# Kernel tuning notes

Measured on AMD Instinct MI355X. Metric: run time of the kernel, lower is better.

## Reference

```python
import jax, jax.numpy as jnp
import numpy as np

PAD_IDX = 0  # tgt_dict.stoi[PAD_WORD]
TLEN, BATCH, SLEN, CVOCAB = 64, 32, 128, 64
D, VOCAB = 1024, 50257


def setup_inputs() -> dict:
    key = jax.random.key(0)
    ks = jax.random.split(key, 7)
    hidden = jax.random.normal(ks[0], (TLEN * BATCH, D), dtype=jnp.float32)
    # attention distribution over source positions (rows sum to 1)
    attn = jax.nn.softmax(jax.random.normal(ks[1], (TLEN * BATCH, SLEN), dtype=jnp.float32), axis=-1)
    # sparse one-hot indicator: each source position maps to one extended-vocab slot
    src_idx = jax.random.randint(ks[2], (SLEN, BATCH), 0, CVOCAB)
    src_map = jax.nn.one_hot(src_idx, CVOCAB, dtype=jnp.float32)  # [slen, batch, cvocab]
    W_gen = jax.random.normal(ks[3], (VOCAB, D), dtype=jnp.float32) * 0.02
    b_gen = jnp.zeros((VOCAB,), dtype=jnp.float32)
    W_copy = jax.random.normal(ks[4], (1, D), dtype=jnp.float32) * 0.02
    b_copy = jnp.zeros((1,), dtype=jnp.float32)
    return {"hidden": hidden, "attn": attn, "src_map": src_map,
            "W_gen": W_gen, "b_gen": b_gen, "W_copy": W_copy, "b_copy": b_copy}


def reference(hidden, attn, src_map, W_gen, b_gen, W_copy, b_copy):
    slen, batch, cvocab = src_map.shape
    # p_softmax over tgt dict, with PAD masked to -inf before softmax
    logits = hidden @ W_gen.T + b_gen                      # [N, vocab]
    logits = logits.at[:, PAD_IDX].set(-jnp.inf)
    prob = jax.nn.softmax(logits, axis=-1)                 # [N, vocab]
    # copy gate p(z)
    p_copy = jax.nn.sigmoid(hidden @ W_copy.T + b_copy)    # [N, 1]
    out_prob = prob * (1.0 - p_copy)                       # [N, vocab]
    mul_attn = attn * p_copy                               # [N, slen]
    # torch flattening is tlen-major: view(-1, batch, slen) -> [tlen, batch, slen]
    mul_attn = mul_attn.reshape(-1, batch, slen)
    # bmm against sparse one-hot indicator: [tlen,batch,slen] x [slen,batch,cvocab]
    copy_prob = jnp.einsum('tbs,sbc->tbc', mul_attn, src_map)
    copy_prob = copy_prob.reshape(-1, cvocab)              # [N, cvocab]
    return jnp.concatenate([out_prob, copy_prob], axis=1)  # [N, vocab+cvocab]
```

## Files before the change

### kernel.cpp

```cpp
#include <hip/hip_runtime.h>
#include <hip/hip_bf16.h>

#define VOCAB 50257
#define CVOCAB 64
#define OUTW (VOCAB + CVOCAB)
#define DDIM 1024
#define NROWS 2048
#define SLEN 128
#define NVT 393
#define NVT2 197
#define VOCABP2 (NVT2 * 256)

typedef __attribute__((ext_vector_type(8))) short bf16x8;
typedef __attribute__((ext_vector_type(4))) float f32x4;

__device__ __forceinline__ unsigned short f2bf(float f) {
  union { float f; unsigned u; } x; x.f = f;
  unsigned r = x.u + 0x7FFFu + ((x.u >> 16) & 1u);
  return (unsigned short)(r >> 16);
}

__device__ __forceinline__ unsigned char f2e4m3(float f) {
  unsigned u = __float_as_uint(f);
  unsigned s = (u >> 24) & 0x80u;
  float a = __uint_as_float(u & 0x7FFFFFFFu);
  if (!(a < 448.f)) a = 448.f;
  if (a < 0.015625f) {
    int q = (int)rintf(a * 512.f);
    return (unsigned char)(s | (unsigned)q);
  }
  unsigned b = __float_as_uint(a);
  unsigned lsb = (b >> 20) & 1u;
  b += 0x0007FFFFu + lsb;
  int e = (int)((b >> 23) & 0xFF) - 127;
  unsigned m = (b >> 20) & 7u;
  return (unsigned char)(s | ((unsigned)(e + 7) << 3) | m);
}

__device__ __forceinline__ unsigned pack_e4m3x4(float a, float b, float c, float d) {
#if __has_builtin(__builtin_amdgcn_cvt_pk_fp8_f32)
  int r = __builtin_amdgcn_cvt_pk_fp8_f32(a, b, 0, false);
  r = __builtin_amdgcn_cvt_pk_fp8_f32(c, d, r, true);
  return (unsigned)r;
#else
  return (unsigned)f2e4m3(a) | ((unsigned)f2e4m3(b) << 8) |
         ((unsigned)f2e4m3(c) << 16) | ((unsigned)f2e4m3(d) << 24);
#endif
}

__device__ __forceinline__ void gload_lds16(const void* g, void* l) {
  __builtin_amdgcn_global_load_lds((const __attribute__((address_space(1))) void*)g,
                                   (__attribute__((address_space(3))) void*)l, 16, 0, 0);
}

__global__ __launch_bounds__(256) void k_pcopy(const float* __restrict__ hidden,
                                               const float* __restrict__ Wc,
                                               const float* __restrict__ bc,
                                               float* __restrict__ pc) {
  int n = blockIdx.x * 4 + (threadIdx.x >> 6);
  int lane = threadIdx.x & 63;
  const float4* h = (const float4*)(hidden + (size_t)n * DDIM);
  const float4* w = (const float4*)Wc;
  float s = 0.0f;
  for (int i = lane; i < DDIM / 4; i += 64) {
    float4 a = h[i], b = w[i];
    s += a.x * b.x + a.y * b.y + a.z * b.z + a.w * b.w;
  }
  #pragma unroll
  for (int m = 1; m < 64; m <<= 1) s += __shfl_xor(s, m);
  if (lane == 0) pc[n] = 1.0f / (1.0f + __expf(-(s + bc[0])));
}

__global__ __launch_bounds__(256) void k_cvtA8(const float* __restrict__ src,
                                               unsigned char* __restrict__ dst) {
  int i = blockIdx.x * 256 + threadIdx.x;
  float4 v = *(const float4*)(src + (size_t)i * 4);
  *(unsigned*)(dst + (size_t)i * 4) = pack_e4m3x4(v.x, v.y, v.z, v.w);
}

__global__ __launch_bounds__(256) void k_cvtW8(const float* __restrict__ Wg,
                                               unsigned char* __restrict__ Wf8) {
  int row = blockIdx.x;
  int t = threadIdx.x;
  unsigned r = 0;
  if (row < VOCAB) {
    float4 v = *(const float4*)(Wg + (size_t)row * DDIM + t * 4);
    r = pack_e4m3x4(v.x * 64.f, v.y * 64.f, v.z * 64.f, v.w * 64.f);
  }
  *(unsigned*)(Wf8 + (size_t)row * DDIM + t * 4) = r;
}

template<int OM>
__global__ __launch_bounds__(512, 2) void k_gemm8(const unsigned char* __restrict__ A,
                                                  const unsigned char* __restrict__ W,
                                                  const float* __restrict__ bg,
                                                  float* __restrict__ out,
                                                  unsigned short* __restrict__ ebuf,
                                                  float* __restrict__ partial) {
  __shared__ __align__(16) unsigned char sA[2][2][256 * 32];
  __shared__ __align__(16) unsigned char sB[2][2][256 * 32];

  const int tid = threadIdx.x;
  const int lane = tid & 63;
  const int w = tid >> 6;
  const int wr = w >> 2, wn = w & 3;
  const int lrow = lane & 15, kgrp = lane >> 4;

  int swz = (blockIdx.x & 7) * 197 + (blockIdx.x >> 3);
  const int mt = swz & 7, vt = swz >> 3;
  const int m0 = mt * 256;
  const int v0 = vt * 256;

  const int srow = tid >> 1, sc16 = tid & 1;
  const int c16s = sc16 ^ ((srow >> 2) & 1);

  #define STAGE_A(t, s) \
    gload_lds16(A + (size_t)(m0 + srow) * DDIM + (t) * 64 + (s) * 32 + c16s * 16, \
                &sA[(t) & 1][s][(size_t)tid * 16]);
  #define STAGE_B(t, s) \
    gload_lds16(W + (size_t)(v0 + srow) * DDIM + (t) * 64 + (s) * 32 + c16s * 16, \
                &sB[(t) & 1][s][(size_t)tid * 16]);

  int aoff[8], boff[4];
  #pragma unroll
  for (int rf = 0; rf < 8; rf++) {
    int row = wr * 128 + rf * 16 + lrow;
    aoff[rf] = row * 32 + (((kgrp >> 1) ^ ((row >> 2) & 1)) << 4) + ((kgrp & 1) << 3);
  }
  #pragma unroll
  for (int cf = 0; cf < 4; cf++) {
    int row = wn * 64 + cf * 16 + lrow;
    boff[cf] = row * 32 + (((kgrp >> 1) ^ ((row >> 2) & 1)) << 4) + ((kgrp & 1) << 3);
  }

  f32x4 acc[8][4] = {};

  STAGE_A(0, 0); STAGE_B(0, 0);
  STAGE_A(0, 1); STAGE_B(0, 1);
  STAGE_A(1, 0); STAGE_B(1, 0);
  asm volatile("s_waitcnt vmcnt(4)" ::: "memory");
  __builtin_amdgcn_s_barrier();

  #define PHASE2(t, sg, STAGE_STMT, WAIT_STMT) { \
    const int _buf = (t) & 1; \
    unsigned long af[8], bfr[4]; \
    const unsigned char* pa = &sA[_buf][sg][0]; \
    const unsigned char* pb = &sB[_buf][sg][0]; \
    _Pragma("unroll") \
    for (int rf = 0; rf < 8; rf++) \
      af[rf] = *(const unsigned long*)(pa + aoff[rf]); \
    _Pragma("unroll") \
    for (int cf = 0; cf < 4; cf++) \
      bfr[cf] = *(const unsigned long*)(pb + boff[cf]); \
    STAGE_STMT; \
    __builtin_amdgcn_s_setprio(1); \
    _Pragma("unroll") \
    for (int rf = 0; rf < 8; rf++) \
      _Pragma("unroll") \
      for (int cf = 0; cf < 4; cf++) \
        acc[rf][cf] = __builtin_amdgcn_mfma_f32_16x16x32_fp8_fp8( \
            (long)af[rf], (long)bfr[cf], acc[rf][cf], 0, 0, 0); \
    __builtin_amdgcn_s_setprio(0); \
    WAIT_STMT; \
    __builtin_amdgcn_s_barrier(); \
  }

  for (int t = 0; t < 16; t++) {
    PHASE2(t, 0,
      { if (t < 15) { STAGE_A(t + 1, 1); STAGE_B(t + 1, 1); } },
      { if (t < 15) { asm volatile("s_waitcnt vmcnt(4)" ::: "memory"); }
        else        { asm volatile("s_waitcnt vmcnt(0)" ::: "memory"); } });
    PHASE2(t, 1,
      { if (t < 14) { STAGE_A(t + 2, 0); STAGE_B(t + 2, 0); } },
      { if (t < 14)       { asm volatile("s_waitcnt vmcnt(4)" ::: "memory"); }
        else if (t == 14) { asm volatile("s_waitcnt vmcnt(2)" ::: "memory"); } });
  }

  asm volatile("s_waitcnt vmcnt(0)" ::: "memory");
  __syncthreads();
  float* psum = (float*)&sA[0][0][0];

  const float INV = 0.015625f;
  float bgv[4];
  int vcol[4];
  #pragma unroll
  for (int cf = 0; cf < 4; cf++) {
    vcol[cf] = v0 + wn * 64 + cf * 16 + lrow;
    bgv[cf] = (vcol[cf] < VOCAB) ? bg[vcol[cf]] : 0.0f;
  }
  #pragma unroll
  for (int a = 0; a < 8; a++) {
    #pragma unroll
    for (int r = 0; r < 4; r++) {
      int lr = wr * 128 + a * 16 + kgrp * 4 + r;
      int row = m0 + lr;
      float s = 0.0f;
      #pragma unroll
      for (int cf = 0; cf < 4; cf++) {
        int v = vcol[cf];
        float e = 0.0f;
        if (v < VOCAB && v != 0) e = __expf(acc[a][cf][r] * INV + bgv[cf]);
        if (OM == 0) {
          if (v < VOCAB) out[(size_t)row * OUTW + v] = e;
        } else {
          if (v < VOCAB) ebuf[(size_t)row * VOCABP2 + v + (row & 3)] = f2bf(e);
        }
        s += e;
      }
      s += __shfl_xor(s, 1); s += __shfl_xor(s, 2);
      s += __shfl_xor(s, 4); s += __shfl_xor(s, 8);
      if (lrow == 0) psum[wn * 256 + lr] = s;
    }
  }
  __syncthreads();
  if (tid < 256)
    partial[(size_t)vt * NROWS + m0 + tid] =
        psum[tid] + psum[256 + tid] + psum[512 + tid] + psum[768 + tid];
  #undef PHASE2
  #undef STAGE_A
  #undef STAGE_B
}

__global__ __launch_bounds__(256) void k_gemm(const float* __restrict__ hidden,
                                              const float* __restrict__ Wg,
                                              const float* __restrict__ bg,
                                              float* __restrict__ out,
                                              float* __restrict__ partial) {
  __shared__ __align__(16) unsigned char smemA[128 * 64 * 2];
  __shared__ __align__(16) unsigned char smemB[128 * 64 * 2];
  __shared__ float psum[2][128];

  const int tid = threadIdx.x;
  const int lane = tid & 63;
  const int wid = tid >> 6;
  const int wr = wid >> 1, wc = wid & 1;
  const int lrow = lane & 15, kgrp = lane >> 4;
  const int m0 = blockIdx.x * 128;
  const int vt = blockIdx.y;
  const int v0 = vt * 128;

  f32x4 acc[4][4] = {};

  for (int kt = 0; kt < 16; kt++) {
    const int k0 = kt * 64;
    #pragma unroll
    for (int i = 0; i < 8; i++) {
      int f = i * 256 + tid;
      int row = f >> 4;
      int kq = (f & 15) << 2;
      float4 v = *(const float4*)(hidden + (size_t)(m0 + row) * DDIM + k0 + kq);
      ushort4 h;
      h.x = f2bf(v.x); h.y = f2bf(v.y); h.z = f2bf(v.z); h.w = f2bf(v.w);
      *(ushort4*)(smemA + row * 128 + ((kq << 1) ^ ((row & 7) << 4))) = h;
    }
    #pragma unroll
    for (int i = 0; i < 8; i++) {
      int f = i * 256 + tid;
      int row = f >> 4;
      int kq = (f & 15) << 2;
      float4 v = make_float4(0.f, 0.f, 0.f, 0.f);
      if (v0 + row < VOCAB)
        v = *(const float4*)(Wg + (size_t)(v0 + row) * DDIM + k0 + kq);
      ushort4 h;
      h.x = f2bf(v.x); h.y = f2bf(v.y); h.z = f2bf(v.z); h.w = f2bf(v.w);
      *(ushort4*)(smemB + row * 128 + ((kq << 1) ^ ((row & 7) << 4))) = h;
    }
    __syncthreads();
    #pragma unroll
    for (int ks = 0; ks < 2; ks++) {
      const int kb = (ks * 32 + kgrp * 8) * 2;
      bf16x8 af[4], bfr[4];
      #pragma unroll
      for (int i = 0; i < 4; i++) {
        int ar = wr * 64 + i * 16 + lrow;
        af[i] = *(const bf16x8*)(smemA + ar * 128 + (kb ^ ((ar & 7) << 4)));
        int br = wc * 64 + i * 16 + lrow;
        bfr[i] = *(const bf16x8*)(smemB + br * 128 + (kb ^ ((br & 7) << 4)));
      }
      #pragma unroll
      for (int i = 0; i < 4; i++)
        #pragma unroll
        for (int j = 0; j < 4; j++)
          acc[i][j] = __builtin_amdgcn_mfma_f32_16x16x32_bf16(af[i], bfr[j], acc[i][j], 0, 0, 0);
    }
    __syncthreads();
  }

  float bgv[4];
  int vcol[4];
  #pragma unroll
  for (int j = 0; j < 4; j++) {
    vcol[j] = v0 + wc * 64 + j * 16 + lrow;
    bgv[j] = (vcol[j] < VOCAB) ? bg[vcol[j]] : 0.0f;
  }
  #pragma unroll
  for (int i = 0; i < 4; i++) {
    #pragma unroll
    for (int r = 0; r < 4; r++) {
      int row = m0 + wr * 64 + i * 16 + kgrp * 4 + r;
      float s = 0.0f;
      #pragma unroll
      for (int j = 0; j < 4; j++) {
        int v = vcol[j];
        float e = 0.0f;
        if (v < VOCAB && v != 0) e = __expf(acc[i][j][r] + bgv[j]);
        if (v < VOCAB) out[(size_t)row * OUTW + v] = e;
        s += e;
      }
      s += __shfl_xor(s, 1); s += __shfl_xor(s, 2);
      s += __shfl_xor(s, 4); s += __shfl_xor(s, 8);
      if ((lane & 15) == 0) psum[wc][wr * 64 + i * 16 + kgrp * 4 + r] = s;
    }
  }
  __syncthreads();
  if (tid < 128)
    partial[(size_t)vt * NROWS + m0 + tid] = psum[0][tid] + psum[1][tid];
}

__global__ __launch_bounds__(256) void k_reduce(const float* __restrict__ partial,
                                                const float* __restrict__ pc,
                                                float* __restrict__ scale, int nvt) {
  int n = blockIdx.x * 256 + threadIdx.x;
  float s = 0.0f;
  for (int t = 0; t < nvt; t++) s += partial[(size_t)t * NROWS + n];
  scale[n] = (1.0f - pc[n]) / s;
}

__global__ __launch_bounds__(256) void k_scale(float* __restrict__ out,
                                               const float* __restrict__ scale) {
  int n = blockIdx.x;
  float sc = scale[n];
  size_t base = (size_t)n * OUTW;
  int off = (int)((4 - (base & 3)) & 3);
  for (int c = threadIdx.x; c < off; c += 256) out[base + c] *= sc;
  int nv = (VOCAB - off) >> 2;
  f32x4* p = (f32x4*)(out + base + off);
  for (int i = threadIdx.x; i < nv; i += 256) {
    f32x4 v = p[i];
    v *= sc;
    __builtin_nontemporal_store(v, &p[i]);
  }
  for (int c = off + (nv << 2) + threadIdx.x; c < VOCAB; c += 256) out[base + c] *= sc;
}

__global__ __launch_bounds__(256) void k_scale2(const unsigned short* __restrict__ ebuf,
                                                const float* __restrict__ scale,
                                                float* __restrict__ out) {
  int n = blockIdx.x;
  float sc = scale[n];
  const int shift = n & 3;
  const int off = (4 - shift) & 3;
  const unsigned short* er = ebuf + (size_t)n * VOCABP2 + shift;
  float* orow = out + (size_t)n * OUTW;
  for (int c = threadIdx.x; c < off; c += 256)
    orow[c] = __uint_as_float((unsigned)er[c] << 16) * sc;
  int nv = (VOCAB - off) >> 2;
  for (int i = threadIdx.x; i < nv; i += 256) {
    int c = off + i * 4;
    ushort4 v = *(const ushort4*)(er + c);
    f32x4 f;
    f.x = __uint_as_float((unsigned)v.x << 16) * sc;
    f.y = __uint_as_float((unsigned)v.y << 16) * sc;
    f.z = __uint_as_float((unsigned)v.z << 16) * sc;
    f.w = __uint_as_float((unsigned)v.w << 16) * sc;
    __builtin_nontemporal_store(f, (f32x4*)(orow + c));
  }
  for (int c = off + (nv << 2) + threadIdx.x; c < VOCAB; c += 256)
    orow[c] = __uint_as_float((unsigned)er[c] << 16) * sc;
}

__global__ __launch_bounds__(64) void k_copy(const float* __restrict__ attn,
                                             const float* __restrict__ src_map,
                                             const float* __restrict__ pc,
                                             float* __restrict__ out) {
  int n = blockIdx.x;
  int c = threadIdx.x;
  int b = n & 31;
  __shared__ float arow[SLEN];
  arow[c] = attn[(size_t)n * SLEN + c];
  arow[c + 64] = attn[(size_t)n * SLEN + 64 + c];
  __syncthreads();
  float s = 0.0f;
  for (int sp = 0; sp < SLEN; sp++)
    s += arow[sp] * src_map[((size_t)sp * 32 + b) * CVOCAB + c];
  out[(size_t)n * OUTW + VOCAB + c] = s * pc[n];
}

extern "C" void kernel_launch(void* const* d_in, const int* in_sizes, int n_in,
                              void* d_out, int out_size, void* d_ws, size_t ws_size,
                              hipStream_t stream) {
  const float* hidden = (const float*)d_in[0];
  const float* attn   = (const float*)d_in[1];
  const float* srcmap = (const float*)d_in[2];
  const float* Wg     = (const float*)d_in[3];
  const float* bg     = (const float*)d_in[4];
  const float* Wc     = (const float*)d_in[5];
  const float* bc     = (const float*)d_in[6];
  float* out = (float*)d_out;

  char* ws = (char*)d_ws;
  float* pc      = (float*)ws;
  float* scale   = (float*)(ws + 8192);
  float* partial = (float*)(ws + 16384);
  size_t partEnd = 16384 + (size_t)NVT * NROWS * 4;
  unsigned char* A8 = (unsigned char*)(ws + partEnd);
  size_t aEnd = partEnd + (size_t)NROWS * DDIM;
  unsigned char* W8 = (unsigned char*)(ws + aEnd);
  size_t wEnd = aEnd + (size_t)VOCABP2 * DDIM;
  unsigned short* ebuf = (unsigned short*)(ws + wEnd);
  size_t need1 = wEnd;
  size_t need2 = wEnd + (size_t)NROWS * VOCABP2 * 2;

  k_pcopy<<<NROWS / 4, 256, 0, stream>>>(hidden, Wc, bc, pc);
  if (ws_size >= need1) {
    k_cvtA8<<<(NROWS * DDIM / 4) / 256, 256, 0, stream>>>(hidden, A8);
    k_cvtW8<<<VOCABP2, 256, 0, stream>>>(Wg, W8);
    if (ws_size >= need2) {
      k_gemm8<1><<<8 * NVT2, 512, 0, stream>>>(A8, W8, bg, out, ebuf, partial);
      k_reduce<<<NROWS / 256, 256, 0, stream>>>(partial, pc, scale, NVT2);
      k_scale2<<<NROWS, 256, 0, stream>>>(ebuf, scale, out);
    } else {
      k_gemm8<0><<<8 * NVT2, 512, 0, stream>>>(A8, W8, bg, out, ebuf, partial);
      k_reduce<<<NROWS / 256, 256, 0, stream>>>(partial, pc, scale, NVT2);
      k_scale<<<NROWS, 256, 0, stream>>>(out, scale);
    }
  } else {
    k_gemm<<<dim3(NROWS / 128, NVT), 256, 0, stream>>>(hidden, Wg, bg, out, partial);
    k_reduce<<<NROWS / 256, 256, 0, stream>>>(partial, pc, scale, NVT);
    k_scale<<<NROWS, 256, 0, stream>>>(out, scale);
  }
  k_copy<<<NROWS, 64, 0, stream>>>(attn, srcmap, pc, out);
}
```

Before: 487.0 us.

## Replace direct global-to-LDS loads with register-staged padded LDS tiles in fp8 GEMM

The fp8 GEMM main loop no longer uses global_load_lds with XOR-swizzled half-tiles. It loads each 64-wide K slice into registers, issues both 32-K MFMA sub-steps, then writes the registers into a padded LDS buffer (row stride 72) and syncs once per K step. Launch bounds are raised to ask for 4 blocks per CU, and the softmax partial sums get their own LDS array instead of reusing the A tile. This trades the async LDS DMA for explicit register staging and more waves per CU. The extra VGPR pressure under the tighter launch bound could cause spills, and the larger LDS footprint may not actually allow higher occupancy.

```diff
diff --git a/kernel.cpp b/kernel.cpp
--- a/kernel.cpp
+++ b/kernel.cpp
@@ -10,9 +10,11 @@
 #define NVT 393
 #define NVT2 197
 #define VOCABP2 (NVT2 * 256)
+#define RSTRIDE 72
 
 typedef __attribute__((ext_vector_type(8))) short bf16x8;
 typedef __attribute__((ext_vector_type(4))) float f32x4;
+typedef __attribute__((ext_vector_type(2))) unsigned long long u64x2;
 
 __device__ __forceinline__ unsigned short f2bf(float f) {
   union { float f; unsigned u; } x; x.f = f;
@@ -46,11 +48,6 @@
   return (unsigned)f2e4m3(a) | ((unsigned)f2e4m3(b) << 8) |
          ((unsigned)f2e4m3(c) << 16) | ((unsigned)f2e4m3(d) << 24);
 #endif
-}
-
-__device__ __forceinline__ void gload_lds16(const void* g, void* l) {
-  __builtin_amdgcn_global_load_lds((const __attribute__((address_space(1))) void*)g,
-                                   (__attribute__((address_space(3))) void*)l, 16, 0, 0);
 }
 
 __global__ __launch_bounds__(256) void k_pcopy(const float* __restrict__ hidden,
@@ -91,14 +88,15 @@
 }
 
 template<int OM>
-__global__ __launch_bounds__(512, 2) void k_gemm8(const unsigned char* __restrict__ A,
+__global__ __launch_bounds__(512, 4) void k_gemm8(const unsigned char* __restrict__ A,
                                                   const unsigned char* __restrict__ W,
                                                   const float* __restrict__ bg,
                                                   float* __restrict__ out,
                                                   unsigned short* __restrict__ ebuf,
                                                   float* __restrict__ partial) {
-  __shared__ __align__(16) unsigned char sA[2][2][256 * 32];
-  __shared__ __align__(16) unsigned char sB[2][2][256 * 32];
+  __shared__ __align__(16) unsigned char sA[2][256 * RSTRIDE];
+  __shared__ __align__(16) unsigned char sB[2][256 * RSTRIDE];
+  __shared__ float psum[1024];
 
   const int tid = threadIdx.x;
   const int lane = tid & 63;
@@ -111,74 +109,86 @@
   const int m0 = mt * 256;
   const int v0 = vt * 256;
 
-  const int srow = tid >> 1, sc16 = tid & 1;
-  const int c16s = sc16 ^ ((srow >> 2) & 1);
-
-  #define STAGE_A(t, s) \
-    gload_lds16(A + (size_t)(m0 + srow) * DDIM + (t) * 64 + (s) * 32 + c16s * 16, \
-                &sA[(t) & 1][s][(size_t)tid * 16]);
-  #define STAGE_B(t, s) \
-    gload_lds16(W + (size_t)(v0 + srow) * DDIM + (t) * 64 + (s) * 32 + c16s * 16, \
-                &sB[(t) & 1][s][(size_t)tid * 16]);
+  const int srow = tid >> 2, scol = (tid & 3) * 16;
+  const size_t gA0 = (size_t)(m0 + srow) * DDIM + scol;
+  const size_t gA1 = gA0 + (size_t)128 * DDIM;
+  const size_t gW0 = (size_t)(v0 + srow) * DDIM + scol;
+  const size_t gW1 = gW0 + (size_t)128 * DDIM;
+  const int l0 = srow * RSTRIDE + scol;
+  const int l1 = l0 + 128 * RSTRIDE;
 
   int aoff[8], boff[4];
   #pragma unroll
-  for (int rf = 0; rf < 8; rf++) {
-    int row = wr * 128 + rf * 16 + lrow;
-    aoff[rf] = row * 32 + (((kgrp >> 1) ^ ((row >> 2) & 1)) << 4) + ((kgrp & 1) << 3);
-  }
-  #pragma unroll
-  for (int cf = 0; cf < 4; cf++) {
-    int row = wn * 64 + cf * 16 + lrow;
-    boff[cf] = row * 32 + (((kgrp >> 1) ^ ((row >> 2) & 1)) << 4) + ((kgrp & 1) << 3);
-  }
+  for (int rf = 0; rf < 8; rf++)
+    aoff[rf] = (wr * 128 + rf * 16 + lrow) * RSTRIDE + kgrp * 8;
+  #pragma unroll
+  for (int cf = 0; cf < 4; cf++)
+    boff[cf] = (wn * 64 + cf * 16 + lrow) * RSTRIDE + kgrp * 8;
 
   f32x4 acc[8][4] = {};
 
-  STAGE_A(0, 0); STAGE_B(0, 0);
-  STAGE_A(0, 1); STAGE_B(0, 1);
-  STAGE_A(1, 0); STAGE_B(1, 0);
-  asm volatile("s_waitcnt vmcnt(4)" ::: "memory");
+  u64x2 ra0, ra1, rb0, rb1;
+
+  #define LOADT(t) { \
+    ra0 = *(const u64x2*)(A + gA0 + (t) * 64); \
+    ra1 = *(const u64x2*)(A + gA1 + (t) * 64); \
+    rb0 = *(const u64x2*)(W + gW0 + (t) * 64); \
+    rb1 = *(const u64x2*)(W + gW1 + (t) * 64); \
+  }
+  #define WRITET(buf) { \
+    unsigned char* da = &sA[buf][0]; \
+    unsigned char* db = &sB[buf][0]; \
+    *(unsigned long long*)(da + l0)     = ra0[0]; \
+    *(unsigned long long*)(da + l0 + 8) = ra0[1]; \
+    *(unsigned long long*)(da + l1)     = ra1[0]; \
+    *(unsigned long long*)(da + l1 + 8) = ra1[1]; \
+    *(unsigned long long*)(db + l0)     = rb0[0]; \
+    *(unsigned long long*)(db + l0 + 8) = rb0[1]; \
+    *(unsigned long long*)(db + l1)     = rb1[0]; \
+    *(unsigned long long*)(db + l1 + 8) = rb1[1]; \
+  }
+
+  LOADT(0);
+  WRITET(0);
+  asm volatile("s_waitcnt lgkmcnt(0)" ::: "memory");
   __builtin_amdgcn_s_barrier();
 
-  #define PHASE2(t, sg, STAGE_STMT, WAIT_STMT) { \
-    const int _buf = (t) & 1; \
-    unsigned long af[8], bfr[4]; \
-    const unsigned char* pa = &sA[_buf][sg][0]; \
-    const unsigned char* pb = &sB[_buf][sg][0]; \
-    _Pragma("unroll") \
-    for (int rf = 0; rf < 8; rf++) \
-      af[rf] = *(const unsigned long*)(pa + aoff[rf]); \
-    _Pragma("unroll") \
-    for (int cf = 0; cf < 4; cf++) \
-      bfr[cf] = *(const unsigned long*)(pb + boff[cf]); \
-    STAGE_STMT; \
-    __builtin_amdgcn_s_setprio(1); \
-    _Pragma("unroll") \
-    for (int rf = 0; rf < 8; rf++) \
-      _Pragma("unroll") \
-      for (int cf = 0; cf < 4; cf++) \
-        acc[rf][cf] = __builtin_amdgcn_mfma_f32_16x16x32_fp8_fp8( \
-            (long)af[rf], (long)bfr[cf], acc[rf][cf], 0, 0, 0); \
-    __builtin_amdgcn_s_setprio(0); \
-    WAIT_STMT; \
-    __builtin_amdgcn_s_barrier(); \
-  }
-
   for (int t = 0; t < 16; t++) {
-    PHASE2(t, 0,
-      { if (t < 15) { STAGE_A(t + 1, 1); STAGE_B(t + 1, 1); } },
-      { if (t < 15) { asm volatile("s_waitcnt vmcnt(4)" ::: "memory"); }
-        else        { asm volatile("s_waitcnt vmcnt(0)" ::: "memory"); } });
-    PHASE2(t, 1,
-      { if (t < 14) { STAGE_A(t + 2, 0); STAGE_B(t + 2, 0); } },
-      { if (t < 14)       { asm volatile("s_waitcnt vmcnt(4)" ::: "memory"); }
-        else if (t == 14) { asm volatile("s_waitcnt vmcnt(2)" ::: "memory"); } });
-  }
-
-  asm volatile("s_waitcnt vmcnt(0)" ::: "memory");
-  __syncthreads();
-  float* psum = (float*)&sA[0][0][0];
+    const unsigned char* pa = &sA[t & 1][0];
+    const unsigned char* pb = &sB[t & 1][0];
+    unsigned long long a0[8], b0[4];
+    #pragma unroll
+    for (int rf = 0; rf < 8; rf++) a0[rf] = *(const unsigned long long*)(pa + aoff[rf]);
+    #pragma unroll
+    for (int cf = 0; cf < 4; cf++) b0[cf] = *(const unsigned long long*)(pb + boff[cf]);
+    if (t < 15) LOADT(t + 1);
+    __builtin_amdgcn_s_setprio(1);
+    #pragma unroll
+    for (int rf = 0; rf < 8; rf++)
+      #pragma unroll
+      for (int cf = 0; cf < 4; cf++)
+        acc[rf][cf] = __builtin_amdgcn_mfma_f32_16x16x32_fp8_fp8(
+            (long)a0[rf], (long)b0[cf], acc[rf][cf], 0, 0, 0);
+    __builtin_amdgcn_s_setprio(0);
+    unsigned long long a1[8], b1[4];
+    #pragma unroll
+    for (int rf = 0; rf < 8; rf++) a1[rf] = *(const unsigned long long*)(pa + aoff[rf] + 32);
+    #pragma unroll
+    for (int cf = 0; cf < 4; cf++) b1[cf] = *(const unsigned long long*)(pb + boff[cf] + 32);
+    __builtin_amdgcn_s_setprio(1);
+    #pragma unroll
+    for (int rf = 0; rf < 8; rf++)
+      #pragma unroll
+      for (int cf = 0; cf < 4; cf++)
+        acc[rf][cf] = __builtin_amdgcn_mfma_f32_16x16x32_fp8_fp8(
+            (long)a1[rf], (long)b1[cf], acc[rf][cf], 0, 0, 0);
+    __builtin_amdgcn_s_setprio(0);
+    if (t < 15) WRITET((t + 1) & 1);
+    asm volatile("s_waitcnt lgkmcnt(0)" ::: "memory");
+    __builtin_amdgcn_s_barrier();
+  }
+  #undef LOADT
+  #undef WRITET
 
   const float INV = 0.015625f;
   float bgv[4];
@@ -216,9 +226,6 @@
   if (tid < 256)
     partial[(size_t)vt * NROWS + m0 + tid] =
         psum[tid] + psum[256 + tid] + psum[512 + tid] + psum[768 + tid];
-  #undef PHASE2
-  #undef STAGE_A
-  #undef STAGE_B
 }
 
 __global__ __launch_bounds__(256) void k_gemm(const float* __restrict__ hidden,
```

After: 1.872 ms. +284.4%, slower.

## Pre-swizzle W into MFMA fragment layout and load B directly to registers

Applied to the files above, without the earlier changes.

The weight conversion kernel now writes FP8 weights in a fragment-packed layout per 256x64 tile, so the GEMM loads B operands straight from global memory into registers and skips LDS for them. The A operand is permuted in k during conversion so each lane reads 16 contiguous bytes covering two MFMA k-steps. A is staged through a padded-stride LDS buffer using register prefetch instead of direct global-to-LDS loads. This is meant to cut LDS traffic and bank conflicts, at the cost of a slower LDS-transposing weight conversion with byte-wise scalar FP8 packing, and B loads that are exposed to global latency.

```diff
diff --git a/kernel.cpp b/kernel.cpp
--- a/kernel.cpp
+++ b/kernel.cpp
@@ -10,9 +10,11 @@
 #define NVT 393
 #define NVT2 197
 #define VOCABP2 (NVT2 * 256)
+#define RSTRIDE 80
 
 typedef __attribute__((ext_vector_type(8))) short bf16x8;
 typedef __attribute__((ext_vector_type(4))) float f32x4;
+typedef __attribute__((ext_vector_type(2))) unsigned long long u64x2;
 
 __device__ __forceinline__ unsigned short f2bf(float f) {
   union { float f; unsigned u; } x; x.f = f;
@@ -46,11 +48,6 @@
   return (unsigned)f2e4m3(a) | ((unsigned)f2e4m3(b) << 8) |
          ((unsigned)f2e4m3(c) << 16) | ((unsigned)f2e4m3(d) << 24);
 #endif
-}
-
-__device__ __forceinline__ void gload_lds16(const void* g, void* l) {
-  __builtin_amdgcn_global_load_lds((const __attribute__((address_space(1))) void*)g,
-                                   (__attribute__((address_space(3))) void*)l, 16, 0, 0);
 }
 
 __global__ __launch_bounds__(256) void k_pcopy(const float* __restrict__ hidden,
@@ -74,31 +71,52 @@
 __global__ __launch_bounds__(256) void k_cvtA8(const float* __restrict__ src,
                                                unsigned char* __restrict__ dst) {
   int i = blockIdx.x * 256 + threadIdx.x;
-  float4 v = *(const float4*)(src + (size_t)i * 4);
-  *(unsigned*)(dst + (size_t)i * 4) = pack_e4m3x4(v.x, v.y, v.z, v.w);
-}
-
-__global__ __launch_bounds__(256) void k_cvtW8(const float* __restrict__ Wg,
-                                               unsigned char* __restrict__ Wf8) {
-  int row = blockIdx.x;
+  int p = i * 4;
+  int row = p >> 10, q = p & 1023;
+  int kt = q >> 6, r = q & 63;
+  int sk = (kt << 6) + ((r >> 3) & 1) * 32 + ((r >> 4) << 3) + (r & 7);
+  float4 v = *(const float4*)(src + ((size_t)row << 10) + sk);
+  *(unsigned*)(dst + (size_t)p) = pack_e4m3x4(v.x, v.y, v.z, v.w);
+}
+
+__global__ __launch_bounds__(256) void k_cvtW8F(const float* __restrict__ Wg,
+                                                unsigned char* __restrict__ Wf) {
+  __shared__ unsigned char ls[256 * 72];
+  int bid = blockIdx.x;
+  int vt = bid >> 4, kt = bid & 15;
   int t = threadIdx.x;
-  unsigned r = 0;
-  if (row < VOCAB) {
-    float4 v = *(const float4*)(Wg + (size_t)row * DDIM + t * 4);
-    r = pack_e4m3x4(v.x * 64.f, v.y * 64.f, v.z * 64.f, v.w * 64.f);
-  }
-  *(unsigned*)(Wf8 + (size_t)row * DDIM + t * 4) = r;
+  int wave = t >> 6, lane = t & 63;
+  int v0 = vt * 256, k0 = kt * 64;
+  for (int rr = 0; rr < 64; rr++) {
+    int row = wave * 64 + rr;
+    int colg = v0 + row;
+    float f = (colg < VOCAB) ? Wg[(size_t)colg * DDIM + k0 + lane] * 64.f : 0.f;
+    ls[row * 72 + lane] = f2e4m3(f);
+  }
+  __syncthreads();
+  size_t base = (size_t)bid * 16384;
+  #pragma unroll
+  for (int ii = 0; ii < 8; ii++) {
+    int p = t * 64 + ii * 8;
+    int f = p >> 9;
+    int l = (p >> 3) & 63;
+    int s = f >> 4, j = f & 15;
+    int col = j * 16 + (l & 15);
+    int kl = s * 32 + ((l >> 4) << 3);
+    *(unsigned long long*)(Wf + base + p) =
+        *(const unsigned long long*)(ls + col * 72 + kl);
+  }
 }
 
 template<int OM>
 __global__ __launch_bounds__(512, 2) void k_gemm8(const unsigned char* __restrict__ A,
-                                                  const unsigned char* __restrict__ W,
+                                                  const unsigned char* __restrict__ Wf,
                                                   const float* __restrict__ bg,
                                                   float* __restrict__ out,
                                                   unsigned short* __restrict__ ebuf,
                                                   float* __restrict__ partial) {
-  __shared__ __align__(16) unsigned char sA[2][2][256 * 32];
-  __shared__ __align__(16) unsigned char sB[2][2][256 * 32];
+  __shared__ __align__(16) unsigned char sA[2][256 * RSTRIDE];
+  __shared__ float psum[1024];
 
   const int tid = threadIdx.x;
   const int lane = tid & 63;
@@ -111,74 +129,75 @@
   const int m0 = mt * 256;
   const int v0 = vt * 256;
 
-  const int srow = tid >> 1, sc16 = tid & 1;
-  const int c16s = sc16 ^ ((srow >> 2) & 1);
-
-  #define STAGE_A(t, s) \
-    gload_lds16(A + (size_t)(m0 + srow) * DDIM + (t) * 64 + (s) * 32 + c16s * 16, \
-                &sA[(t) & 1][s][(size_t)tid * 16]);
-  #define STAGE_B(t, s) \
-    gload_lds16(W + (size_t)(v0 + srow) * DDIM + (t) * 64 + (s) * 32 + c16s * 16, \
-                &sB[(t) & 1][s][(size_t)tid * 16]);
-
-  int aoff[8], boff[4];
-  #pragma unroll
-  for (int rf = 0; rf < 8; rf++) {
-    int row = wr * 128 + rf * 16 + lrow;
-    aoff[rf] = row * 32 + (((kgrp >> 1) ^ ((row >> 2) & 1)) << 4) + ((kgrp & 1) << 3);
-  }
-  #pragma unroll
-  for (int cf = 0; cf < 4; cf++) {
-    int row = wn * 64 + cf * 16 + lrow;
-    boff[cf] = row * 32 + (((kgrp >> 1) ^ ((row >> 2) & 1)) << 4) + ((kgrp & 1) << 3);
-  }
+  const int srow = tid >> 2, scol = (tid & 3) * 16;
+  const size_t gA0 = (size_t)(m0 + srow) * DDIM + scol;
+  const size_t gA1 = gA0 + (size_t)128 * DDIM;
+  const int l0 = srow * RSTRIDE + scol;
+  const int l1 = l0 + 128 * RSTRIDE;
+
+  int aoff[8];
+  #pragma unroll
+  for (int rf = 0; rf < 8; rf++)
+    aoff[rf] = (wr * 128 + rf * 16 + lrow) * RSTRIDE + kgrp * 16;
 
   f32x4 acc[8][4] = {};
-
-  STAGE_A(0, 0); STAGE_B(0, 0);
-  STAGE_A(0, 1); STAGE_B(0, 1);
-  STAGE_A(1, 0); STAGE_B(1, 0);
-  asm volatile("s_waitcnt vmcnt(4)" ::: "memory");
-  __builtin_amdgcn_s_barrier();
-
-  #define PHASE2(t, sg, STAGE_STMT, WAIT_STMT) { \
-    const int _buf = (t) & 1; \
-    unsigned long af[8], bfr[4]; \
-    const unsigned char* pa = &sA[_buf][sg][0]; \
-    const unsigned char* pb = &sB[_buf][sg][0]; \
+  u64x2 ra0, ra1;
+  unsigned long long bA[8], bB[8];
+
+  #define LOADT(t) { \
+    ra0 = *(const u64x2*)(A + gA0 + (t) * 64); \
+    ra1 = *(const u64x2*)(A + gA1 + (t) * 64); \
+  }
+  #define WRITET(buf) { \
+    unsigned char* da = &sA[buf][0]; \
+    *(u64x2*)(da + l0) = ra0; \
+    *(u64x2*)(da + l1) = ra1; \
+  }
+  #define LOADB(dst, t) { \
+    const unsigned char* wb = Wf + ((((size_t)vt * 16 + (t)) * 32 + wn * 4) << 9) + (lane << 3); \
     _Pragma("unroll") \
-    for (int rf = 0; rf < 8; rf++) \
-      af[rf] = *(const unsigned long*)(pa + aoff[rf]); \
+    for (int q = 0; q < 8; q++) \
+      dst[q] = *(const unsigned long long*)(wb + (((q >> 2) * 16 + (q & 3)) << 9)); \
+  }
+  #define TILE(t, BU, BN, PF) { \
+    const unsigned char* pa = &sA[(t) & 1][0]; \
+    u64x2 av[8]; \
     _Pragma("unroll") \
-    for (int cf = 0; cf < 4; cf++) \
-      bfr[cf] = *(const unsigned long*)(pb + boff[cf]); \
-    STAGE_STMT; \
+    for (int rf = 0; rf < 8; rf++) av[rf] = *(const u64x2*)(pa + aoff[rf]); \
+    if (PF) { LOADB(BN, (t) + 1); LOADT((t) + 1); } \
     __builtin_amdgcn_s_setprio(1); \
     _Pragma("unroll") \
     for (int rf = 0; rf < 8; rf++) \
       _Pragma("unroll") \
       for (int cf = 0; cf < 4; cf++) \
         acc[rf][cf] = __builtin_amdgcn_mfma_f32_16x16x32_fp8_fp8( \
-            (long)af[rf], (long)bfr[cf], acc[rf][cf], 0, 0, 0); \
+            (long)av[rf][0], (long)BU[cf], acc[rf][cf], 0, 0, 0); \
+    _Pragma("unroll") \
+    for (int rf = 0; rf < 8; rf++) \
+      _Pragma("unroll") \
+      for (int cf = 0; cf < 4; cf++) \
+        acc[rf][cf] = __builtin_amdgcn_mfma_f32_16x16x32_fp8_fp8( \
+            (long)av[rf][1], (long)BU[4 + cf], acc[rf][cf], 0, 0, 0); \
     __builtin_amdgcn_s_setprio(0); \
-    WAIT_STMT; \
+    if (PF) WRITET(((t) + 1) & 1); \
+    asm volatile("s_waitcnt lgkmcnt(0)" ::: "memory"); \
     __builtin_amdgcn_s_barrier(); \
   }
 
-  for (int t = 0; t < 16; t++) {
-    PHASE2(t, 0,
-      { if (t < 15) { STAGE_A(t + 1, 1); STAGE_B(t + 1, 1); } },
-      { if (t < 15) { asm volatile("s_waitcnt vmcnt(4)" ::: "memory"); }
-        else        { asm volatile("s_waitcnt vmcnt(0)" ::: "memory"); } });
-    PHASE2(t, 1,
-      { if (t < 14) { STAGE_A(t + 2, 0); STAGE_B(t + 2, 0); } },
-      { if (t < 14)       { asm volatile("s_waitcnt vmcnt(4)" ::: "memory"); }
-        else if (t == 14) { asm volatile("s_waitcnt vmcnt(2)" ::: "memory"); } });
-  }
-
-  asm volatile("s_waitcnt vmcnt(0)" ::: "memory");
-  __syncthreads();
-  float* psum = (float*)&sA[0][0][0];
+  LOADB(bA, 0);
+  LOADT(0);
+  WRITET(0);
+  asm volatile("s_waitcnt lgkmcnt(0)" ::: "memory");
+  __builtin_amdgcn_s_barrier();
+
+  for (int t = 0; t < 16; t += 2) {
+    TILE(t, bA, bB, true);
+    TILE(t + 1, bB, bA, (t + 2 < 16));
+  }
+  #undef TILE
+  #undef LOADB
+  #undef WRITET
+  #undef LOADT
 
   const float INV = 0.015625f;
   float bgv[4];
@@ -216,9 +235,6 @@
   if (tid < 256)
     partial[(size_t)vt * NROWS + m0 + tid] =
         psum[tid] + psum[256 + tid] + psum[512 + tid] + psum[768 + tid];
-  #undef PHASE2
-  #undef STAGE_A
-  #undef STAGE_B
 }
 
 __global__ __launch_bounds__(256) void k_gemm(const float* __restrict__ hidden,
@@ -405,7 +421,7 @@
   size_t partEnd = 16384 + (size_t)NVT * NROWS * 4;
   unsigned char* A8 = (unsigned char*)(ws + partEnd);
   size_t aEnd = partEnd + (size_t)NROWS * DDIM;
-  unsigned char* W8 = (unsigned char*)(ws + aEnd);
+  unsigned char* Wf = (unsigned char*)(ws + aEnd);
   size_t wEnd = aEnd + (size_t)VOCABP2 * DDIM;
   unsigned short* ebuf = (unsigned short*)(ws + wEnd);
   size_t need1 = wEnd;
@@ -414,13 +430,13 @@
   k_pcopy<<<NROWS / 4, 256, 0, stream>>>(hidden, Wc, bc, pc);
   if (ws_size >= need1) {
     k_cvtA8<<<(NROWS * DDIM / 4) / 256, 256, 0, stream>>>(hidden, A8);
-    k_cvtW8<<<VOCABP2, 256, 0, stream>>>(Wg, W8);
+    k_cvtW8F<<<NVT2 * 16, 256, 0, stream>>>(Wg, Wf);
     if (ws_size >= need2) {
-      k_gemm8<1><<<8 * NVT2, 512, 0, stream>>>(A8, W8, bg, out, ebuf, partial);
+      k_gemm8<1><<<8 * NVT2, 512, 0, stream>>>(A8, Wf, bg, out, ebuf, partial);
       k_reduce<<<NROWS / 256, 256, 0, stream>>>(partial, pc, scale, NVT2);
       k_scale2<<<NROWS, 256, 0, stream>>>(ebuf, scale, out);
     } else {
-      k_gemm8<0><<<8 * NVT2, 512, 0, stream>>>(A8, W8, bg, out, ebuf, partial);
+      k_gemm8<0><<<8 * NVT2, 512, 0, stream>>>(A8, Wf, bg, out, ebuf, partial);
       k_reduce<<<NROWS / 256, 256, 0, stream>>>(partial, pc, scale, NVT2);
       k_scale<<<NROWS, 256, 0, stream>>>(out, scale);
     }
```

New measurement: 511.7 us. 5.1% more time.

## Pre-swizzle FP8 operands into MFMA fragment order and drop LDS staging in GEMM

Applied to the files above, without the earlier changes.

The FP8 conversion kernels now write hidden and W_gen in a tiled layout that matches the per-lane MFMA fragment order. This lets the new GEMM kernel load operands straight from global memory into registers with simple 8-byte loads, with no LDS staging or barriers. Tiles shrink to 64x64 per wave (256-thread blocks, 64-wide vocab tiles), so the partial-sum array grows to 788 tiles per row and each wave writes its own row sums. The trade is more global and L2 traffic from less reuse per block, in exchange for no LDS round trips and no synchronisation.

```diff
diff --git a/kernel.cpp b/kernel.cpp
--- a/kernel.cpp
+++ b/kernel.cpp
@@ -8,8 +8,9 @@
 #define NROWS 2048
 #define SLEN 128
 #define NVT 393
-#define NVT2 197
-#define VOCABP2 (NVT2 * 256)
+#define VOCABP2 50432
+#define NVT64 788
+#define NAS 32
 
 typedef __attribute__((ext_vector_type(8))) short bf16x8;
 typedef __attribute__((ext_vector_type(4))) float f32x4;
@@ -46,11 +47,6 @@
   return (unsigned)f2e4m3(a) | ((unsigned)f2e4m3(b) << 8) |
          ((unsigned)f2e4m3(c) << 16) | ((unsigned)f2e4m3(d) << 24);
 #endif
-}
-
-__device__ __forceinline__ void gload_lds16(const void* g, void* l) {
-  __builtin_amdgcn_global_load_lds((const __attribute__((address_space(1))) void*)g,
-                                   (__attribute__((address_space(3))) void*)l, 16, 0, 0);
 }
 
 __global__ __launch_bounds__(256) void k_pcopy(const float* __restrict__ hidden,
@@ -71,135 +67,108 @@
   if (lane == 0) pc[n] = 1.0f / (1.0f + __expf(-(s + bc[0])));
 }
 
-__global__ __launch_bounds__(256) void k_cvtA8(const float* __restrict__ src,
-                                               unsigned char* __restrict__ dst) {
-  int i = blockIdx.x * 256 + threadIdx.x;
-  float4 v = *(const float4*)(src + (size_t)i * 4);
-  *(unsigned*)(dst + (size_t)i * 4) = pack_e4m3x4(v.x, v.y, v.z, v.w);
-}
-
-__global__ __launch_bounds__(256) void k_cvtW8(const float* __restrict__ Wg,
-                                               unsigned char* __restrict__ Wf8) {
-  int row = blockIdx.x;
-  int t = threadIdx.x;
-  unsigned r = 0;
-  if (row < VOCAB) {
-    float4 v = *(const float4*)(Wg + (size_t)row * DDIM + t * 4);
-    r = pack_e4m3x4(v.x * 64.f, v.y * 64.f, v.z * 64.f, v.w * 64.f);
-  }
-  *(unsigned*)(Wf8 + (size_t)row * DDIM + t * 4) = r;
+__global__ __launch_bounds__(256) void k_cvt8F(const float* __restrict__ src,
+                                               unsigned char* __restrict__ dst,
+                                               int validRows, float scale) {
+  __shared__ unsigned char ls[64 * 72];
+  const int bid = blockIdx.x;
+  const int strip = bid >> 4, kt = bid & 15;
+  const int t = threadIdx.x;
+  const int r = t >> 2, part = t & 3;
+  const int row = strip * 64 + r;
+  const int k0 = kt * 64 + part * 16;
+  #pragma unroll
+  for (int j = 0; j < 4; j++) {
+    unsigned pk = 0;
+    if (row < validRows) {
+      float4 v = *(const float4*)(src + (size_t)row * DDIM + k0 + j * 4);
+      pk = pack_e4m3x4(v.x * scale, v.y * scale, v.z * scale, v.w * scale);
+    }
+    *(unsigned*)(ls + r * 72 + part * 16 + j * 4) = pk;
+  }
+  __syncthreads();
+  size_t base = (size_t)bid * 4096;
+  #pragma unroll
+  for (int ii = 0; ii < 2; ii++) {
+    int p = ii * 2048 + t * 8;
+    int s = ii, rfl = t >> 6, l = t & 63;
+    *(unsigned long long*)(dst + base + p) =
+        *(const unsigned long long*)(ls + (rfl * 16 + (l & 15)) * 72 + s * 32 + ((l >> 4) << 3));
+  }
 }
 
 template<int OM>
-__global__ __launch_bounds__(512, 2) void k_gemm8(const unsigned char* __restrict__ A,
-                                                  const unsigned char* __restrict__ W,
+__global__ __launch_bounds__(256, 2) void k_gemm9(const unsigned char* __restrict__ Af,
+                                                  const unsigned char* __restrict__ Wf,
                                                   const float* __restrict__ bg,
                                                   float* __restrict__ out,
                                                   unsigned short* __restrict__ ebuf,
                                                   float* __restrict__ partial) {
-  __shared__ __align__(16) unsigned char sA[2][2][256 * 32];
-  __shared__ __align__(16) unsigned char sB[2][2][256 * 32];
-
   const int tid = threadIdx.x;
   const int lane = tid & 63;
   const int w = tid >> 6;
-  const int wr = w >> 2, wn = w & 3;
   const int lrow = lane & 15, kgrp = lane >> 4;
 
-  int swz = (blockIdx.x & 7) * 197 + (blockIdx.x >> 3);
-  const int mt = swz & 7, vt = swz >> 3;
-  const int m0 = mt * 256;
-  const int v0 = vt * 256;
-
-  const int srow = tid >> 1, sc16 = tid & 1;
-  const int c16s = sc16 ^ ((srow >> 2) & 1);
-
-  #define STAGE_A(t, s) \
-    gload_lds16(A + (size_t)(m0 + srow) * DDIM + (t) * 64 + (s) * 32 + c16s * 16, \
-                &sA[(t) & 1][s][(size_t)tid * 16]);
-  #define STAGE_B(t, s) \
-    gload_lds16(W + (size_t)(v0 + srow) * DDIM + (t) * 64 + (s) * 32 + c16s * 16, \
-                &sB[(t) & 1][s][(size_t)tid * 16]);
-
-  int aoff[8], boff[4];
-  #pragma unroll
-  for (int rf = 0; rf < 8; rf++) {
-    int row = wr * 128 + rf * 16 + lrow;
-    aoff[rf] = row * 32 + (((kgrp >> 1) ^ ((row >> 2) & 1)) << 4) + ((kgrp & 1) << 3);
-  }
-  #pragma unroll
-  for (int cf = 0; cf < 4; cf++) {
-    int row = wn * 64 + cf * 16 + lrow;
-    boff[cf] = row * 32 + (((kgrp >> 1) ^ ((row >> 2) & 1)) << 4) + ((kgrp & 1) << 3);
-  }
-
-  f32x4 acc[8][4] = {};
-
-  STAGE_A(0, 0); STAGE_B(0, 0);
-  STAGE_A(0, 1); STAGE_B(0, 1);
-  STAGE_A(1, 0); STAGE_B(1, 0);
-  asm volatile("s_waitcnt vmcnt(4)" ::: "memory");
-  __builtin_amdgcn_s_barrier();
-
-  #define PHASE2(t, sg, STAGE_STMT, WAIT_STMT) { \
-    const int _buf = (t) & 1; \
-    unsigned long af[8], bfr[4]; \
-    const unsigned char* pa = &sA[_buf][sg][0]; \
-    const unsigned char* pb = &sB[_buf][sg][0]; \
+  int swz = (blockIdx.x & 7) * 788 + (blockIdx.x >> 3);
+  const int mtb = swz & 7, vt = swz >> 3;
+  const int astrip = mtb * 4 + w;
+  const int m0 = astrip * 64;
+  const int v0 = vt * 64;
+
+  const unsigned char* Ab = Af + ((size_t)astrip * 16) * 4096 + lane * 8;
+  const unsigned char* Bb = Wf + ((size_t)vt * 16) * 4096 + lane * 8;
+
+  f32x4 acc[4][4] = {};
+  unsigned long long aA[8], bA[8], aB[8], bB[8];
+
+  #define LOADF(afr, bfr, kt) { \
     _Pragma("unroll") \
-    for (int rf = 0; rf < 8; rf++) \
-      af[rf] = *(const unsigned long*)(pa + aoff[rf]); \
+    for (int q = 0; q < 8; q++) { \
+      afr[q] = *(const unsigned long long*)(Ab + (kt) * 4096 + q * 512); \
+      bfr[q] = *(const unsigned long long*)(Bb + (kt) * 4096 + q * 512); \
+    } \
+  }
+  #define MTILE(afr, bfr) { \
     _Pragma("unroll") \
-    for (int cf = 0; cf < 4; cf++) \
-      bfr[cf] = *(const unsigned long*)(pb + boff[cf]); \
-    STAGE_STMT; \
-    __builtin_amdgcn_s_setprio(1); \
-    _Pragma("unroll") \
-    for (int rf = 0; rf < 8; rf++) \
+    for (int s = 0; s < 2; s++) \
       _Pragma("unroll") \
-      for (int cf = 0; cf < 4; cf++) \
-        acc[rf][cf] = __builtin_amdgcn_mfma_f32_16x16x32_fp8_fp8( \
-            (long)af[rf], (long)bfr[cf], acc[rf][cf], 0, 0, 0); \
-    __builtin_amdgcn_s_setprio(0); \
-    WAIT_STMT; \
-    __builtin_amdgcn_s_barrier(); \
-  }
-
-  for (int t = 0; t < 16; t++) {
-    PHASE2(t, 0,
-      { if (t < 15) { STAGE_A(t + 1, 1); STAGE_B(t + 1, 1); } },
-      { if (t < 15) { asm volatile("s_waitcnt vmcnt(4)" ::: "memory"); }
-        else        { asm volatile("s_waitcnt vmcnt(0)" ::: "memory"); } });
-    PHASE2(t, 1,
-      { if (t < 14) { STAGE_A(t + 2, 0); STAGE_B(t + 2, 0); } },
-      { if (t < 14)       { asm volatile("s_waitcnt vmcnt(4)" ::: "memory"); }
-        else if (t == 14) { asm volatile("s_waitcnt vmcnt(2)" ::: "memory"); } });
-  }
-
-  asm volatile("s_waitcnt vmcnt(0)" ::: "memory");
-  __syncthreads();
-  float* psum = (float*)&sA[0][0][0];
+      for (int rf = 0; rf < 4; rf++) \
+        _Pragma("unroll") \
+        for (int cf = 0; cf < 4; cf++) \
+          acc[rf][cf] = __builtin_amdgcn_mfma_f32_16x16x32_fp8_fp8( \
+              (long)afr[s * 4 + rf], (long)bfr[s * 4 + cf], acc[rf][cf], 0, 0, 0); \
+  }
+
+  LOADF(aA, bA, 0);
+  #pragma unroll
+  for (int kt = 0; kt < 16; kt += 2) {
+    if (kt + 1 < 16) LOADF(aB, bB, kt + 1);
+    MTILE(aA, bA);
+    if (kt + 2 < 16) LOADF(aA, bA, kt + 2);
+    MTILE(aB, bB);
+  }
+  #undef MTILE
+  #undef LOADF
 
   const float INV = 0.015625f;
   float bgv[4];
   int vcol[4];
   #pragma unroll
   for (int cf = 0; cf < 4; cf++) {
-    vcol[cf] = v0 + wn * 64 + cf * 16 + lrow;
+    vcol[cf] = v0 + cf * 16 + lrow;
     bgv[cf] = (vcol[cf] < VOCAB) ? bg[vcol[cf]] : 0.0f;
   }
   #pragma unroll
-  for (int a = 0; a < 8; a++) {
+  for (int rf = 0; rf < 4; rf++) {
     #pragma unroll
     for (int r = 0; r < 4; r++) {
-      int lr = wr * 128 + a * 16 + kgrp * 4 + r;
-      int row = m0 + lr;
+      int row = m0 + rf * 16 + kgrp * 4 + r;
       float s = 0.0f;
       #pragma unroll
       for (int cf = 0; cf < 4; cf++) {
         int v = vcol[cf];
         float e = 0.0f;
-        if (v < VOCAB && v != 0) e = __expf(acc[a][cf][r] * INV + bgv[cf]);
+        if (v < VOCAB && v != 0) e = __expf(acc[rf][cf][r] * INV + bgv[cf]);
         if (OM == 0) {
           if (v < VOCAB) out[(size_t)row * OUTW + v] = e;
         } else {
@@ -209,16 +178,9 @@
       }
       s += __shfl_xor(s, 1); s += __shfl_xor(s, 2);
       s += __shfl_xor(s, 4); s += __shfl_xor(s, 8);
-      if (lrow == 0) psum[wn * 256 + lr] = s;
-    }
-  }
-  __syncthreads();
-  if (tid < 256)
-    partial[(size_t)vt * NROWS + m0 + tid] =
-        psum[tid] + psum[256 + tid] + psum[512 + tid] + psum[768 + tid];
-  #undef PHASE2
-  #undef STAGE_A
-  #undef STAGE_B
+      if (lrow == 0) partial[(size_t)vt * NROWS + row] = s;
+    }
+  }
 }
 
 __global__ __launch_bounds__(256) void k_gemm(const float* __restrict__ hidden,
@@ -402,26 +364,26 @@
   float* pc      = (float*)ws;
   float* scale   = (float*)(ws + 8192);
   float* partial = (float*)(ws + 16384);
-  size_t partEnd = 16384 + (size_t)NVT * NROWS * 4;
-  unsigned char* A8 = (unsigned char*)(ws + partEnd);
-  size_t aEnd = partEnd + (size_t)NROWS * DDIM;
-  unsigned char* W8 = (unsigned char*)(ws + aEnd);
-  size_t wEnd = aEnd + (size_t)VOCABP2 * DDIM;
+  size_t partEnd = 16384 + (size_t)NVT64 * NROWS * 4;
+  unsigned char* A8F = (unsigned char*)(ws + partEnd);
+  size_t aEnd = partEnd + (size_t)NAS * 16 * 4096;
+  unsigned char* Wf = (unsigned char*)(ws + aEnd);
+  size_t wEnd = aEnd + (size_t)NVT64 * 16 * 4096;
   unsigned short* ebuf = (unsigned short*)(ws + wEnd);
   size_t need1 = wEnd;
   size_t need2 = wEnd + (size_t)NROWS * VOCABP2 * 2;
 
   k_pcopy<<<NROWS / 4, 256, 0, stream>>>(hidden, Wc, bc, pc);
   if (ws_size >= need1) {
-    k_cvtA8<<<(NROWS * DDIM / 4) / 256, 256, 0, stream>>>(hidden, A8);
-    k_cvtW8<<<VOCABP2, 256, 0, stream>>>(Wg, W8);
+    k_cvt8F<<<NAS * 16, 256, 0, stream>>>(hidden, A8F, NROWS, 1.0f);
+    k_cvt8F<<<NVT64 * 16, 256, 0, stream>>>(Wg, Wf, VOCAB, 64.0f);
     if (ws_size >= need2) {
-      k_gemm8<1><<<8 * NVT2, 512, 0, stream>>>(A8, W8, bg, out, ebuf, partial);
-      k_reduce<<<NROWS / 256, 256, 0, stream>>>(partial, pc, scale, NVT2);
+      k_gemm9<1><<<8 * NVT64, 256, 0, stream>>>(A8F, Wf, bg, out, ebuf, partial);
+      k_reduce<<<NROWS / 256, 256, 0, stream>>>(partial, pc, scale, NVT64);
       k_scale2<<<NROWS, 256, 0, stream>>>(ebuf, scale, out);
     } else {
-      k_gemm8<0><<<8 * NVT2, 512, 0, stream>>>(A8, W8, bg, out, ebuf, partial);
-      k_reduce<<<NROWS / 256, 256, 0, stream>>>(partial, pc, scale, NVT2);
+      k_gemm9<0><<<8 * NVT64, 256, 0, stream>>>(A8F, Wf, bg, out, ebuf, partial);
+      k_reduce<<<NROWS / 256, 256, 0, stream>>>(partial, pc, scale, NVT64);
       k_scale<<<NROWS, 256, 0, stream>>>(out, scale);
     }
   } else {
```

Result: slower. 632.3 us (+29.8%).
